# Kernel optimization log

Measured on AMD Instinct MI355X. Metric: run time of the kernel, lower is better.

Reference implementation:

```python
import jax, jax.numpy as jnp
import numpy as np

PATCH = 14  # dinov2 patch size
LN_EPS = 1e-5


def setup_inputs() -> dict:
    key = jax.random.key(0)
    ks = jax.random.split(key, 6)
    Nb, P, E, Hd = 4096, 5476, 1024, 128  # boxes, patches (74*74), embed_dim, hidden_dim
    return {
        "patch_tokens": jax.random.normal(ks[0], (1, P, E), dtype=jnp.float32),
        "bboxes": jax.random.randint(ks[1], (Nb, 4), 0, 1036, dtype=jnp.int32),
        "H": 1036,
        "W": 1036,
        "W1": jax.random.normal(ks[2], (E, Hd), dtype=jnp.float32) * 0.02,
        "b1": jnp.zeros((Hd,), dtype=jnp.float32),
        "gamma": jnp.ones((Hd,), dtype=jnp.float32),
        "beta": jnp.zeros((Hd,), dtype=jnp.float32),
        "W2": jax.random.normal(ks[3], (Hd, Hd), dtype=jnp.float32) * 0.02,
        "b2": jnp.zeros((Hd,), dtype=jnp.float32),
    }


def _roi_pool(patch_tokens, bboxes, H, W):
    """Vectorized equivalent of VisionEncoder.roi_pool_patches.

    patch_tokens: (1, nph*npw, E); bboxes: (Nb, 4) int pixel coords.
    Returns (Nb, E) mean of patch tokens inside each box.
    """
    nph, npw = H // PATCH, W // PATCH
    Nb = bboxes.shape[0]
    x1, y1, x2, y2 = (bboxes[:, 0], bboxes[:, 1], bboxes[:, 2], bboxes[:, 3])
    f32 = jnp.float32
    # int() truncation in torch == astype(int32) for non-negative values
    px1 = (x1.astype(f32) / W * npw).astype(jnp.int32)
    px2 = (x2.astype(f32) / W * npw).astype(jnp.int32)
    py1 = (y1.astype(f32) / H * nph).astype(jnp.int32)
    py2 = (y2.astype(f32) / H * nph).astype(jnp.int32)
    px1 = jnp.clip(px1, 0, npw - 1)
    px2 = jnp.maximum(px1 + 1, jnp.minimum(px2, npw))
    py1 = jnp.clip(py1, 0, nph - 1)
    py2 = jnp.maximum(py1 + 1, jnp.minimum(py2, nph))
    # Box membership masks over the patch grid (ragged gather expressed densely)
    ay = jnp.arange(nph, dtype=jnp.int32)
    ax = jnp.arange(npw, dtype=jnp.int32)
    my = (ay[None, :] >= py1[:, None]) & (ay[None, :] < py2[:, None])  # (Nb, nph)
    mx = (ax[None, :] >= px1[:, None]) & (ax[None, :] < px2[:, None])  # (Nb, npw)
    mask = (my[:, :, None] & mx[:, None, :]).reshape(Nb, nph * npw)
    mask = mask.astype(patch_tokens.dtype)
    counts = mask.sum(axis=-1, keepdims=True)  # always >= 1 by construction
    pooled = (mask @ patch_tokens[0]) / counts  # (Nb, E)
    return pooled


def _projection(x, W1, b1, gamma, beta, W2, b2):
    h = x @ W1 + b1
    mu = h.mean(axis=-1, keepdims=True)
    var = ((h - mu) ** 2).mean(axis=-1, keepdims=True)
    h = (h - mu) * jax.lax.rsqrt(var + LN_EPS) * gamma + beta
    h = jax.nn.relu(h)
    return h @ W2 + b2


def reference(patch_tokens, bboxes, H, W, W1, b1, gamma, beta, W2, b2):
    pooled = _roi_pool(patch_tokens, bboxes, H, W)
    return _projection(pooled, W1, b1, gamma, beta, W2, b2)
```

## Files before the change

### kernel.cpp

```cpp
#include <hip/hip_runtime.h>


#define HD 128
#define SPLITK 8

typedef __attribute__((ext_vector_type(8))) short bf16x8;
typedef __attribute__((ext_vector_type(4))) float f32x4;

__device__ __forceinline__ int decode_dim(const int* p, int fallback) {
    if (p == nullptr) return fallback;
    int vi = *p;
    if (vi >= 1 && vi <= 1000000) return vi;
    float vf = __int_as_float(vi);
    if (vf >= 1.0f && vf <= 1000000.0f) return (int)vf;
    return fallback;
}

__attribute__((noinline, optnone))
__device__ int coord_map(int x, int W, int n) {
    double rd = 1.0 / (double)W;
    float r = (float)rd;
    double qd = (double)x * (double)r;
    float q = (float)qd;
    double pd = (double)q * (double)n;
    float p = (float)pd;
    return (int)p;
}

__device__ __forceinline__ unsigned short bf16_rne(float x) {
    unsigned u = __float_as_uint(x);
    unsigned r = u + 0x7fffu + ((u >> 16) & 1u);
    return (unsigned short)(r >> 16);
}

__global__ __launch_bounds__(256) void split_w1_kernel(
    const float* __restrict__ W1, unsigned short* __restrict__ Whi,
    unsigned short* __restrict__ Wlo, int E)
{
    __shared__ float tile[64][65];
    int t = threadIdx.x;
    int k0 = blockIdx.x * 64, n0 = blockIdx.y * 64;

    int r = t >> 4, c4 = (t & 15) * 4;
#pragma unroll
    for (int i = 0; i < 4; ++i) {
        int kr = r + i * 16;
        *(float4*)&tile[kr][c4] =
            *(const float4*)&W1[(size_t)(k0 + kr) * HD + n0 + c4];
    }
    __syncthreads();

    int nl = t >> 2, kq = (t & 3) * 16;
    unsigned hp[8], lp[8];
#pragma unroll
    for (int j = 0; j < 8; ++j) {
        float x0 = tile[kq + 2 * j][nl];
        float x1 = tile[kq + 2 * j + 1][nl];
        unsigned h0 = bf16_rne(x0);
        unsigned h1 = bf16_rne(x1);
        float l0 = x0 - __uint_as_float(h0 << 16);
        float l1 = x1 - __uint_as_float(h1 << 16);
        hp[j] = h0 | ((unsigned)h1 << 16);
        lp[j] = (unsigned)bf16_rne(l0) | ((unsigned)bf16_rne(l1) << 16);
    }
    size_t off = (size_t)(n0 + nl) * E + k0 + kq;
    *(uint4*)(Whi + off)     = make_uint4(hp[0], hp[1], hp[2], hp[3]);
    *(uint4*)(Whi + off + 8) = make_uint4(hp[4], hp[5], hp[6], hp[7]);
    *(uint4*)(Wlo + off)     = make_uint4(lp[0], lp[1], lp[2], lp[3]);
    *(uint4*)(Wlo + off + 8) = make_uint4(lp[4], lp[5], lp[6], lp[7]);
}

__global__ __launch_bounds__(256) void gemm_u_mfma(
    const float* __restrict__ T, const unsigned short* __restrict__ Whi,
    const unsigned short* __restrict__ Wlo, float* __restrict__ U,
    int P, int E)
{
    int t = threadIdx.x;
    int lane = t & 63;
    int w = t >> 6;
    int row0 = blockIdx.x * 32 + (w & 1) * 16;
    int col0 = (w >> 1) * 64;
    int kchunk = E >> 3;
    int kbase = blockIdx.y * kchunk;
    float* Uo = U + (size_t)blockIdx.y * (size_t)P * HD;

    int lr  = lane & 15;
    int lkq = (lane >> 4) * 8;

    int arow = row0 + lr; if (arow >= P) arow = P - 1;
    const float* ap = T + (size_t)arow * E + kbase + lkq;
    const unsigned short* bh0 = Whi + (size_t)(col0 + lr) * E + kbase + lkq;
    const unsigned short* bl0 = Wlo + (size_t)(col0 + lr) * E + kbase + lkq;

    f32x4 acc[4];
#pragma unroll
    for (int n = 0; n < 4; ++n) acc[n] = (f32x4){0.f, 0.f, 0.f, 0.f};

    float4 ca0 = *(const float4*)(ap);
    float4 ca1 = *(const float4*)(ap + 4);

    for (int kt = 0; kt < kchunk; kt += 32) {
        float4 na0 = ca0, na1 = ca1;
        if (kt + 32 < kchunk) {
            na0 = *(const float4*)(ap + kt + 32);
            na1 = *(const float4*)(ap + kt + 36);
        }
        bf16x8 bhv[4], blv[4];
#pragma unroll
        for (int n = 0; n < 4; ++n) {
            bhv[n] = *(const bf16x8*)(bh0 + (size_t)(n * 16) * E + kt);
            blv[n] = *(const bf16x8*)(bl0 + (size_t)(n * 16) * E + kt);
        }

        float av[8] = {ca0.x, ca0.y, ca0.z, ca0.w, ca1.x, ca1.y, ca1.z, ca1.w};
        bf16x8 ahi, alo;
#pragma unroll
        for (int j = 0; j < 8; ++j) {
            unsigned h = bf16_rne(av[j]);
            ahi[j] = (short)h;
            float l = av[j] - __uint_as_float(h << 16);
            alo[j] = (short)bf16_rne(l);
        }

#pragma unroll
        for (int n = 0; n < 4; ++n) {
            acc[n] = __builtin_amdgcn_mfma_f32_16x16x32_bf16(ahi, bhv[n], acc[n], 0, 0, 0);
            acc[n] = __builtin_amdgcn_mfma_f32_16x16x32_bf16(alo, bhv[n], acc[n], 0, 0, 0);
            acc[n] = __builtin_amdgcn_mfma_f32_16x16x32_bf16(ahi, blv[n], acc[n], 0, 0, 0);
        }
        ca0 = na0; ca1 = na1;
    }

    int cr0 = row0 + (lane >> 4) * 4;
    int cc  = lane & 15;
#pragma unroll
    for (int n = 0; n < 4; ++n) {
#pragma unroll
        for (int r = 0; r < 4; ++r) {
            int p = cr0 + r;
            if (p < P) Uo[(size_t)p * HD + col0 + n * 16 + cc] = acc[n][r];
        }
    }
}

__global__ __launch_bounds__(256) void prefix_x_kernel(
    const float* __restrict__ U, float* __restrict__ S,
    int P, int npw, int nph)
{
    extern __shared__ float tile[];
    int t = threadIdx.x;
    int y = blockIdx.x;
    int ch0 = blockIdx.y * 64;
    size_t ustride = (size_t)P * HD;
    size_t ubase = (size_t)y * npw * HD + ch0;

    int nj = npw * 16;
    for (int j = t; j < nj; j += 256) {
        int x = j >> 4, cq = (j & 15) * 4;
        size_t off = ubase + (size_t)x * HD + cq;
        float4 s = *(const float4*)(U + off);
#pragma unroll
        for (int p = 1; p < SPLITK; ++p) {
            float4 v = *(const float4*)(U + (size_t)p * ustride + off);
            s.x += v.x; s.y += v.y; s.z += v.z; s.w += v.w;
        }
        *(float4*)&tile[x * 64 + cq] = s;
    }
    __syncthreads();

    if (t < 64) {
        int c = t;
        size_t srow = (size_t)(y + 1) * (npw + 1) * HD + ch0;
        S[srow + c] = 0.f;
        float acc = 0.f;
        for (int x = 0; x < npw; ++x) {
            acc += tile[x * 64 + c];
            S[srow + (size_t)(x + 1) * HD + c] = acc;
        }
    }
}

__global__ __launch_bounds__(256) void prefix_y_kernel(
    float* __restrict__ S, int npw, int nph)
{
    extern __shared__ float tile[];
    int t = threadIdx.x;
    int x = blockIdx.x;
    int ch0 = blockIdx.y * 64;
    size_t stride = (size_t)(npw + 1) * HD;
    size_t base = (size_t)x * HD + ch0;

    int nj = nph * 16;
    for (int j = t; j < nj; j += 256) {
        int y = j >> 4, cq = (j & 15) * 4;
        *(float4*)&tile[y * 64 + cq] =
            *(const float4*)(S + base + (size_t)(y + 1) * stride + cq);
    }
    __syncthreads();

    if (t < 64) {
        int c = t;
        S[base + c] = 0.f;
        float acc = 0.f;
        for (int y = 0; y < nph; ++y) {
            acc += tile[y * 64 + c];
            S[base + (size_t)(y + 1) * stride + c] = acc;
        }
    }
}

__global__ __launch_bounds__(256) void pool_proj_kernel(
    const float* __restrict__ S, const int* __restrict__ bboxes,
    const int* __restrict__ pH, const int* __restrict__ pW,
    const float* __restrict__ b1, const float* __restrict__ gamma,
    const float* __restrict__ beta, const float* __restrict__ W2,
    const float* __restrict__ b2, float* __restrict__ out,
    int Nb, int npw, int nph, int fbW, int fbH)
{
    __shared__ float hs[16][HD + 1];
    __shared__ float Bs[32][HD];
    __shared__ float red_s[16][17], red_q[16][17];
    __shared__ int   cI11[16], cI12[16], cI21[16], cI22[16];
    __shared__ float cCnt[16];
    __shared__ float mu_s[16], rs_s[16];

    int t = threadIdx.x;
    int c = t & 127;
    int rh = t >> 7;
    int row0 = blockIdx.x * 16;

    if (t < 16) {
        int b = row0 + t; if (b >= Nb) b = Nb - 1;
        int x1 = bboxes[b * 4 + 0];
        int y1 = bboxes[b * 4 + 1];
        int x2 = bboxes[b * 4 + 2];
        int y2 = bboxes[b * 4 + 3];
        int Wi = decode_dim(pW, fbW);
        int Hi = decode_dim(pH, fbH);
        int px1 = coord_map(x1, Wi, npw);
        int px2 = coord_map(x2, Wi, npw);
        int py1 = coord_map(y1, Hi, nph);
        int py2 = coord_map(y2, Hi, nph);
        px1 = min(max(px1, 0), npw - 1);
        px2 = max(px1 + 1, min(px2, npw));
        py1 = min(max(py1, 0), nph - 1);
        py2 = max(py1 + 1, min(py2, nph));
        int st = npw + 1;
        cI11[t] = (py1 * st + px1) * HD;
        cI12[t] = (py1 * st + px2) * HD;
        cI21[t] = (py2 * st + px1) * HD;
        cI22[t] = (py2 * st + px2) * HD;
        cCnt[t] = (float)((py2 - py1) * (px2 - px1));
    }
    __syncthreads();

    float bias1 = b1[c];
    float hv[8];
#pragma unroll
    for (int r = 0; r < 8; ++r) {
        int row = rh * 8 + r;
        float s = S[cI22[row] + c] - S[cI12[row] + c]
                - S[cI21[row] + c] + S[cI11[row] + c];
        hv[r] = s / cCnt[row] + bias1;
        hs[row][c] = hv[r];
    }
    __syncthreads();

    {
        int sr = t & 15;
        int sg = t >> 4;
        float ps = 0.f, pq = 0.f;
#pragma unroll
        for (int i = 0; i < 8; ++i) {
            float v = hs[sr][sg * 8 + i];
            ps += v; pq += v * v;
        }
        red_s[sr][sg] = ps; red_q[sr][sg] = pq;
    }
    __syncthreads();
    if (t < 16) {
        float s = 0.f, q = 0.f;
#pragma unroll
        for (int i = 0; i < 16; ++i) { s += red_s[t][i]; q += red_q[t][i]; }
        float m = s * (1.0f / HD);
        float v = q * (1.0f / HD) - m * m;
        mu_s[t] = m;
        rs_s[t] = rsqrtf(v + 1e-5f);
    }
    __syncthreads();

    float g = gamma[c], be = beta[c];
#pragma unroll
    for (int r = 0; r < 8; ++r) {
        int row = rh * 8 + r;
        float x = (hv[r] - mu_s[row]) * rs_s[row] * g + be;
        hs[row][c] = fmaxf(x, 0.f);
    }
    __syncthreads();

    float bias2 = b2[c];
    float acc2[8];
#pragma unroll
    for (int r = 0; r < 8; ++r) acc2[r] = bias2;
    for (int k0 = 0; k0 < HD; k0 += 32) {
#pragma unroll
        for (int i = 0; i < 16; ++i) {
            int idx = t + i * 256;
            int kk = idx >> 7, cc = idx & 127;
            Bs[kk][cc] = W2[(size_t)(k0 + kk) * HD + cc];
        }
        __syncthreads();
#pragma unroll
        for (int kk = 0; kk < 32; ++kk) {
            float bv = Bs[kk][c];
#pragma unroll
            for (int r = 0; r < 8; ++r)
                acc2[r] += hs[rh * 8 + r][k0 + kk] * bv;
        }
        __syncthreads();
    }

#pragma unroll
    for (int r = 0; r < 8; ++r) {
        int rg = row0 + rh * 8 + r;
        if (rg < Nb) out[(size_t)rg * HD + c] = acc2[r];
    }
}

extern "C" void kernel_launch(void* const* d_in, const int* in_sizes, int n_in,
                              void* d_out, int out_size, void* d_ws, size_t ws_size,
                              hipStream_t stream) {
    int iT = 0, iB = 1, iH = 2, iW = 3, iW1 = 4, ib1 = 5, ig = 6, ibe = 7,
        iW2 = 8, ib2 = 9;
    bool has_scalars = (n_in >= 10 && in_sizes[2] == 1 && in_sizes[3] == 1);
    if (!has_scalars) { iW1 = 2; ib1 = 3; ig = 4; ibe = 5; iW2 = 6; ib2 = 7; }

    const float* tokens = (const float*)d_in[iT];
    const int*   bboxes = (const int*)d_in[iB];
    const int*   pH     = has_scalars ? (const int*)d_in[iH] : nullptr;
    const int*   pW     = has_scalars ? (const int*)d_in[iW] : nullptr;
    const float* W1     = (const float*)d_in[iW1];
    const float* b1     = (const float*)d_in[ib1];
    const float* gamma  = (const float*)d_in[ig];
    const float* beta   = (const float*)d_in[ibe];
    const float* W2     = (const float*)d_in[iW2];
    const float* b2     = (const float*)d_in[ib2];
    float* out = (float*)d_out;

    int Hd = in_sizes[ib1];
    int E  = in_sizes[iW1] / Hd;
    int Nb = in_sizes[iB] / 4;
    int P  = in_sizes[iT] / E;
    int npw = 1;
    while ((npw + 1) * (npw + 1) <= P) ++npw;
    int nph = P / npw;
    (void)out_size; (void)ws_size;

    float* S = (float*)d_ws;
    size_t s_elems = ((size_t)(nph + 1) * (npw + 1) * HD + 255) & ~(size_t)255;
    float* U = S + s_elems;
    size_t u_elems = (size_t)SPLITK * (size_t)P * HD;
    unsigned short* Whi = (unsigned short*)(U + u_elems);
    unsigned short* Wlo = Whi + (size_t)E * HD;

    split_w1_kernel<<<dim3(E / 64, HD / 64), dim3(256), 0, stream>>>(
        W1, Whi, Wlo, E);

    int mtiles = (P + 31) / 32;
    gemm_u_mfma<<<dim3(mtiles, SPLITK), dim3(256), 0, stream>>>(
        tokens, Whi, Wlo, U, P, E);
    prefix_x_kernel<<<dim3(nph, 2), dim3(256), (size_t)npw * 64 * 4, stream>>>(
        U, S, P, npw, nph);
    prefix_y_kernel<<<dim3(npw + 1, 2), dim3(256), (size_t)nph * 64 * 4, stream>>>(
        S, npw, nph);
    pool_proj_kernel<<<dim3((Nb + 15) / 16), dim3(256), 0, stream>>>(
        S, bboxes, pH, pW, b1, gamma, beta, W2, b2, out, Nb, npw, nph,
        14 * npw, 14 * nph);
}
```

Before: 145.4 us.

## Fuse all stages into one persistent kernel with grid barriers, drop split-K

Replaces the five separate launches (W1 split, split-K GEMM, x-prefix, y-prefix, pool+projection) with one persistent kernel of 256 blocks x 512 threads, separated by software grid barriers built on atomics. The GEMM no longer splits K: each wave computes a full-K 16x64 tile, which removes the 8-way partial buffer and its reduction. The prefix scans run one wave per row or column straight from global memory, with no shared-memory staging. This saves launch overhead and partial-sum traffic, but adds barrier cost and relies on all 256 blocks being co-resident. It also leaves much less parallelism in the GEMM and scan phases (about 686 GEMM tasks and 148 scan tasks for 2048 waves).

New measurement: 302.8 us. 2.08x slower.

```diff
diff --git a/kernel.cpp b/kernel.cpp
--- a/kernel.cpp
+++ b/kernel.cpp
@@ -1,8 +1,9 @@
 #include <hip/hip_runtime.h>
 
 
-#define HD 128
-#define SPLITK 8
+#define HD   128
+#define NBLK 256
+#define NTHR 512
 
 typedef __attribute__((ext_vector_type(8))) short bf16x8;
 typedef __attribute__((ext_vector_type(4))) float f32x4;
@@ -33,297 +34,347 @@
     return (unsigned short)(r >> 16);
 }
 
-__global__ __launch_bounds__(256) void split_w1_kernel(
-    const float* __restrict__ W1, unsigned short* __restrict__ Whi,
-    unsigned short* __restrict__ Wlo, int E)
+__device__ __forceinline__ void gbar(int* cnt, int* gen) {
+    __syncthreads();
+    if (threadIdx.x == 0) {
+        __threadfence();
+        int g = __hip_atomic_load(gen, __ATOMIC_RELAXED,
+                                  __HIP_MEMORY_SCOPE_AGENT);
+        int a = __hip_atomic_fetch_add(cnt, 1, __ATOMIC_ACQ_REL,
+                                       __HIP_MEMORY_SCOPE_AGENT);
+        if (a == NBLK - 1) {
+            __hip_atomic_store(cnt, 0, __ATOMIC_RELAXED,
+                               __HIP_MEMORY_SCOPE_AGENT);
+            __hip_atomic_store(gen, g + 1, __ATOMIC_RELEASE,
+                               __HIP_MEMORY_SCOPE_AGENT);
+        } else {
+            while (__hip_atomic_load(gen, __ATOMIC_RELAXED,
+                                     __HIP_MEMORY_SCOPE_AGENT) == g)
+                __builtin_amdgcn_s_sleep(16);
+        }
+        __threadfence();
+    }
+    __syncthreads();
+}
+
+#define STEP(A0, A1, KT) do {                                               \
+    bf16x8 bhv[4], blv[4];                                                  \
+    _Pragma("unroll")                                                       \
+    for (int n = 0; n < 4; ++n) {                                           \
+        bhv[n] = *(const bf16x8*)(bh0 + (size_t)(n * 16) * E + (KT));       \
+        blv[n] = *(const bf16x8*)(bl0 + (size_t)(n * 16) * E + (KT));       \
+    }                                                                       \
+    float av[8] = {(A0).x, (A0).y, (A0).z, (A0).w,                          \
+                   (A1).x, (A1).y, (A1).z, (A1).w};                         \
+    bf16x8 ahi, alo;                                                        \
+    _Pragma("unroll")                                                       \
+    for (int j = 0; j < 8; ++j) {                                           \
+        unsigned h = bf16_rne(av[j]);                                       \
+        ahi[j] = (short)h;                                                  \
+        float l = av[j] - __uint_as_float(h << 16);                         \
+        alo[j] = (short)bf16_rne(l);                                        \
+    }                                                                       \
+    _Pragma("unroll")                                                       \
+    for (int n = 0; n < 4; ++n) {                                           \
+        acc[n] = __builtin_amdgcn_mfma_f32_16x16x32_bf16(ahi, bhv[n],       \
+                                                         acc[n], 0, 0, 0); \
+        acc[n] = __builtin_amdgcn_mfma_f32_16x16x32_bf16(alo, bhv[n],       \
+                                                         acc[n], 0, 0, 0); \
+        acc[n] = __builtin_amdgcn_mfma_f32_16x16x32_bf16(ahi, blv[n],       \
+                                                         acc[n], 0, 0, 0); \
+    }                                                                       \
+} while (0)
+
+__global__ __launch_bounds__(NTHR, 1) void fused_all(
+    const float* __restrict__ T, const int* __restrict__ bboxes,
+    const int* __restrict__ pH, const int* __restrict__ pW,
+    const float* __restrict__ W1, const float* __restrict__ b1,
+    const float* __restrict__ gamma, const float* __restrict__ beta,
+    const float* __restrict__ W2, const float* __restrict__ b2,
+    float* __restrict__ out,
+    float* S, float* U, unsigned short* Whi, unsigned short* Wlo,
+    int* cnt, int* gen,
+    int P, int E, int Nb, int npw, int nph, int fbW, int fbH)
 {
-    __shared__ float tile[64][65];
-    int t = threadIdx.x;
-    int k0 = blockIdx.x * 64, n0 = blockIdx.y * 64;
-
-    int r = t >> 4, c4 = (t & 15) * 4;
-#pragma unroll
-    for (int i = 0; i < 4; ++i) {
-        int kr = r + i * 16;
-        *(float4*)&tile[kr][c4] =
-            *(const float4*)&W1[(size_t)(k0 + kr) * HD + n0 + c4];
-    }
-    __syncthreads();
-
-    int nl = t >> 2, kq = (t & 3) * 16;
-    unsigned hp[8], lp[8];
-#pragma unroll
-    for (int j = 0; j < 8; ++j) {
-        float x0 = tile[kq + 2 * j][nl];
-        float x1 = tile[kq + 2 * j + 1][nl];
-        unsigned h0 = bf16_rne(x0);
-        unsigned h1 = bf16_rne(x1);
-        float l0 = x0 - __uint_as_float(h0 << 16);
-        float l1 = x1 - __uint_as_float(h1 << 16);
-        hp[j] = h0 | ((unsigned)h1 << 16);
-        lp[j] = (unsigned)bf16_rne(l0) | ((unsigned)bf16_rne(l1) << 16);
-    }
-    size_t off = (size_t)(n0 + nl) * E + k0 + kq;
-    *(uint4*)(Whi + off)     = make_uint4(hp[0], hp[1], hp[2], hp[3]);
-    *(uint4*)(Whi + off + 8) = make_uint4(hp[4], hp[5], hp[6], hp[7]);
-    *(uint4*)(Wlo + off)     = make_uint4(lp[0], lp[1], lp[2], lp[3]);
-    *(uint4*)(Wlo + off + 8) = make_uint4(lp[4], lp[5], lp[6], lp[7]);
-}
-
-__global__ __launch_bounds__(256) void gemm_u_mfma(
-    const float* __restrict__ T, const unsigned short* __restrict__ Whi,
-    const unsigned short* __restrict__ Wlo, float* __restrict__ U,
-    int P, int E)
-{
-    int t = threadIdx.x;
-    int lane = t & 63;
-    int w = t >> 6;
-    int row0 = blockIdx.x * 32 + (w & 1) * 16;
-    int col0 = (w >> 1) * 64;
-    int kchunk = E >> 3;
-    int kbase = blockIdx.y * kchunk;
-    float* Uo = U + (size_t)blockIdx.y * (size_t)P * HD;
-
-    int lr  = lane & 15;
-    int lkq = (lane >> 4) * 8;
-
-    int arow = row0 + lr; if (arow >= P) arow = P - 1;
-    const float* ap = T + (size_t)arow * E + kbase + lkq;
-    const unsigned short* bh0 = Whi + (size_t)(col0 + lr) * E + kbase + lkq;
-    const unsigned short* bl0 = Wlo + (size_t)(col0 + lr) * E + kbase + lkq;
-
-    f32x4 acc[4];
-#pragma unroll
-    for (int n = 0; n < 4; ++n) acc[n] = (f32x4){0.f, 0.f, 0.f, 0.f};
-
-    float4 ca0 = *(const float4*)(ap);
-    float4 ca1 = *(const float4*)(ap + 4);
-
-    for (int kt = 0; kt < kchunk; kt += 32) {
-        float4 na0 = ca0, na1 = ca1;
-        if (kt + 32 < kchunk) {
-            na0 = *(const float4*)(ap + kt + 32);
-            na1 = *(const float4*)(ap + kt + 36);
-        }
-        bf16x8 bhv[4], blv[4];
-#pragma unroll
-        for (int n = 0; n < 4; ++n) {
-            bhv[n] = *(const bf16x8*)(bh0 + (size_t)(n * 16) * E + kt);
-            blv[n] = *(const bf16x8*)(bl0 + (size_t)(n * 16) * E + kt);
-        }
-
-        float av[8] = {ca0.x, ca0.y, ca0.z, ca0.w, ca1.x, ca1.y, ca1.z, ca1.w};
-        bf16x8 ahi, alo;
-#pragma unroll
-        for (int j = 0; j < 8; ++j) {
-            unsigned h = bf16_rne(av[j]);
-            ahi[j] = (short)h;
-            float l = av[j] - __uint_as_float(h << 16);
-            alo[j] = (short)bf16_rne(l);
-        }
-
-#pragma unroll
-        for (int n = 0; n < 4; ++n) {
-            acc[n] = __builtin_amdgcn_mfma_f32_16x16x32_bf16(ahi, bhv[n], acc[n], 0, 0, 0);
-            acc[n] = __builtin_amdgcn_mfma_f32_16x16x32_bf16(alo, bhv[n], acc[n], 0, 0, 0);
-            acc[n] = __builtin_amdgcn_mfma_f32_16x16x32_bf16(ahi, blv[n], acc[n], 0, 0, 0);
-        }
-        ca0 = na0; ca1 = na1;
-    }
-
-    int cr0 = row0 + (lane >> 4) * 4;
-    int cc  = lane & 15;
-#pragma unroll
-    for (int n = 0; n < 4; ++n) {
-#pragma unroll
-        for (int r = 0; r < 4; ++r) {
-            int p = cr0 + r;
-            if (p < P) Uo[(size_t)p * HD + col0 + n * 16 + cc] = acc[n][r];
-        }
-    }
-}
-
-__global__ __launch_bounds__(256) void prefix_x_kernel(
-    const float* __restrict__ U, float* __restrict__ S,
-    int P, int npw, int nph)
-{
-    extern __shared__ float tile[];
-    int t = threadIdx.x;
-    int y = blockIdx.x;
-    int ch0 = blockIdx.y * 64;
-    size_t ustride = (size_t)P * HD;
-    size_t ubase = (size_t)y * npw * HD + ch0;
-
-    int nj = npw * 16;
-    for (int j = t; j < nj; j += 256) {
-        int x = j >> 4, cq = (j & 15) * 4;
-        size_t off = ubase + (size_t)x * HD + cq;
-        float4 s = *(const float4*)(U + off);
-#pragma unroll
-        for (int p = 1; p < SPLITK; ++p) {
-            float4 v = *(const float4*)(U + (size_t)p * ustride + off);
-            s.x += v.x; s.y += v.y; s.z += v.z; s.w += v.w;
-        }
-        *(float4*)&tile[x * 64 + cq] = s;
-    }
-    __syncthreads();
-
-    if (t < 64) {
-        int c = t;
-        size_t srow = (size_t)(y + 1) * (npw + 1) * HD + ch0;
-        S[srow + c] = 0.f;
-        float acc = 0.f;
-        for (int x = 0; x < npw; ++x) {
-            acc += tile[x * 64 + c];
-            S[srow + (size_t)(x + 1) * HD + c] = acc;
-        }
-    }
-}
-
-__global__ __launch_bounds__(256) void prefix_y_kernel(
-    float* __restrict__ S, int npw, int nph)
-{
-    extern __shared__ float tile[];
-    int t = threadIdx.x;
-    int x = blockIdx.x;
-    int ch0 = blockIdx.y * 64;
-    size_t stride = (size_t)(npw + 1) * HD;
-    size_t base = (size_t)x * HD + ch0;
-
-    int nj = nph * 16;
-    for (int j = t; j < nj; j += 256) {
-        int y = j >> 4, cq = (j & 15) * 4;
-        *(float4*)&tile[y * 64 + cq] =
-            *(const float4*)(S + base + (size_t)(y + 1) * stride + cq);
-    }
-    __syncthreads();
-
-    if (t < 64) {
-        int c = t;
-        S[base + c] = 0.f;
-        float acc = 0.f;
-        for (int y = 0; y < nph; ++y) {
-            acc += tile[y * 64 + c];
-            S[base + (size_t)(y + 1) * stride + c] = acc;
-        }
-    }
-}
-
-__global__ __launch_bounds__(256) void pool_proj_kernel(
-    const float* __restrict__ S, const int* __restrict__ bboxes,
-    const int* __restrict__ pH, const int* __restrict__ pW,
-    const float* __restrict__ b1, const float* __restrict__ gamma,
-    const float* __restrict__ beta, const float* __restrict__ W2,
-    const float* __restrict__ b2, float* __restrict__ out,
-    int Nb, int npw, int nph, int fbW, int fbH)
-{
+    __shared__ float sh_tile[64][65];
     __shared__ float hs[16][HD + 1];
     __shared__ float Bs[32][HD];
-    __shared__ float red_s[16][17], red_q[16][17];
+    __shared__ float red_s[16][33], red_q[16][33];
     __shared__ int   cI11[16], cI12[16], cI21[16], cI22[16];
     __shared__ float cCnt[16];
     __shared__ float mu_s[16], rs_s[16];
 
     int t = threadIdx.x;
-    int c = t & 127;
-    int rh = t >> 7;
-    int row0 = blockIdx.x * 16;
-
-    if (t < 16) {
-        int b = row0 + t; if (b >= Nb) b = Nb - 1;
-        int x1 = bboxes[b * 4 + 0];
-        int y1 = bboxes[b * 4 + 1];
-        int x2 = bboxes[b * 4 + 2];
-        int y2 = bboxes[b * 4 + 3];
-        int Wi = decode_dim(pW, fbW);
-        int Hi = decode_dim(pH, fbH);
-        int px1 = coord_map(x1, Wi, npw);
-        int px2 = coord_map(x2, Wi, npw);
-        int py1 = coord_map(y1, Hi, nph);
-        int py2 = coord_map(y2, Hi, nph);
-        px1 = min(max(px1, 0), npw - 1);
-        px2 = max(px1 + 1, min(px2, npw));
-        py1 = min(max(py1, 0), nph - 1);
-        py2 = max(py1 + 1, min(py2, nph));
-        int st = npw + 1;
-        cI11[t] = (py1 * st + px1) * HD;
-        cI12[t] = (py1 * st + px2) * HD;
-        cI21[t] = (py2 * st + px1) * HD;
-        cI22[t] = (py2 * st + px2) * HD;
-        cCnt[t] = (float)((py2 - py1) * (px2 - px1));
-    }
-    __syncthreads();
-
-    float bias1 = b1[c];
-    float hv[8];
-#pragma unroll
-    for (int r = 0; r < 8; ++r) {
-        int row = rh * 8 + r;
-        float s = S[cI22[row] + c] - S[cI12[row] + c]
-                - S[cI21[row] + c] + S[cI11[row] + c];
-        hv[r] = s / cCnt[row] + bias1;
-        hs[row][c] = hv[r];
-    }
-    __syncthreads();
+    int b = blockIdx.x;
+    int w = t >> 6;
+    int lane = t & 63;
 
     {
-        int sr = t & 15;
-        int sg = t >> 4;
-        float ps = 0.f, pq = 0.f;
-#pragma unroll
-        for (int i = 0; i < 8; ++i) {
-            float v = hs[sr][sg * 8 + i];
-            ps += v; pq += v * v;
-        }
-        red_s[sr][sg] = ps; red_q[sr][sg] = pq;
-    }
-    __syncthreads();
-    if (t < 16) {
-        float s = 0.f, q = 0.f;
-#pragma unroll
-        for (int i = 0; i < 16; ++i) { s += red_s[t][i]; q += red_q[t][i]; }
-        float m = s * (1.0f / HD);
-        float v = q * (1.0f / HD) - m * m;
-        mu_s[t] = m;
-        rs_s[t] = rsqrtf(v + 1e-5f);
-    }
-    __syncthreads();
-
-    float g = gamma[c], be = beta[c];
-#pragma unroll
-    for (int r = 0; r < 8; ++r) {
-        int row = rh * 8 + r;
-        float x = (hv[r] - mu_s[row]) * rs_s[row] * g + be;
-        hs[row][c] = fmaxf(x, 0.f);
-    }
-    __syncthreads();
-
-    float bias2 = b2[c];
-    float acc2[8];
-#pragma unroll
-    for (int r = 0; r < 8; ++r) acc2[r] = bias2;
-    for (int k0 = 0; k0 < HD; k0 += 32) {
-#pragma unroll
-        for (int i = 0; i < 16; ++i) {
-            int idx = t + i * 256;
-            int kk = idx >> 7, cc = idx & 127;
-            Bs[kk][cc] = W2[(size_t)(k0 + kk) * HD + cc];
-        }
-        __syncthreads();
-#pragma unroll
-        for (int kk = 0; kk < 32; ++kk) {
-            float bv = Bs[kk][c];
-#pragma unroll
-            for (int r = 0; r < 8; ++r)
-                acc2[r] += hs[rh * 8 + r][k0 + kk] * bv;
-        }
-        __syncthreads();
-    }
-
-#pragma unroll
-    for (int r = 0; r < 8; ++r) {
-        int rg = row0 + rh * 8 + r;
-        if (rg < Nb) out[(size_t)rg * HD + c] = acc2[r];
+        int ntile0 = (E >> 6) * (HD >> 6);
+        for (int tb = b; tb < ntile0; tb += NBLK) {
+            int k0 = (tb >> 1) * 64, n0 = (tb & 1) * 64;
+            if (t < 256) {
+                int r = t >> 4, c4 = (t & 15) * 4;
+#pragma unroll
+                for (int i = 0; i < 4; ++i) {
+                    int kr = r + i * 16;
+                    *(float4*)&sh_tile[kr][c4] =
+                        *(const float4*)&W1[(size_t)(k0 + kr) * HD + n0 + c4];
+                }
+            }
+            __syncthreads();
+            if (t < 256) {
+                int nl = t >> 2, kq = (t & 3) * 16;
+                unsigned hp[8], lp[8];
+#pragma unroll
+                for (int j = 0; j < 8; ++j) {
+                    float x0 = sh_tile[kq + 2 * j][nl];
+                    float x1 = sh_tile[kq + 2 * j + 1][nl];
+                    unsigned h0 = bf16_rne(x0);
+                    unsigned h1 = bf16_rne(x1);
+                    float l0 = x0 - __uint_as_float(h0 << 16);
+                    float l1 = x1 - __uint_as_float(h1 << 16);
+                    hp[j] = h0 | ((unsigned)h1 << 16);
+                    lp[j] = (unsigned)bf16_rne(l0) |
+                            ((unsigned)bf16_rne(l1) << 16);
+                }
+                size_t off = (size_t)(n0 + nl) * E + k0 + kq;
+                *(uint4*)(Whi + off)     = make_uint4(hp[0], hp[1], hp[2], hp[3]);
+                *(uint4*)(Whi + off + 8) = make_uint4(hp[4], hp[5], hp[6], hp[7]);
+                *(uint4*)(Wlo + off)     = make_uint4(lp[0], lp[1], lp[2], lp[3]);
+                *(uint4*)(Wlo + off + 8) = make_uint4(lp[4], lp[5], lp[6], lp[7]);
+            }
+            __syncthreads();
+        }
+    }
+    gbar(cnt, gen);
+
+    {
+        int ntasks = ((P + 15) >> 4) * 2;
+        for (int task = w * NBLK + b; task < ntasks; task += NBLK * 8) {
+            int rt = task >> 1, ch = task & 1;
+            int row0 = rt * 16, col0 = ch * 64;
+            int lr = lane & 15, lkq = (lane >> 4) * 8;
+            int arow = row0 + lr; if (arow >= P) arow = P - 1;
+            const float* ap = T + (size_t)arow * E + lkq;
+            const unsigned short* bh0 = Whi + (size_t)(col0 + lr) * E + lkq;
+            const unsigned short* bl0 = Wlo + (size_t)(col0 + lr) * E + lkq;
+
+            f32x4 acc[4];
+#pragma unroll
+            for (int n = 0; n < 4; ++n) acc[n] = (f32x4){0.f, 0.f, 0.f, 0.f};
+
+            float4 pa0 = *(const float4*)(ap);
+            float4 pa1 = *(const float4*)(ap + 4);
+            float4 qa0 = *(const float4*)(ap + 32);
+            float4 qa1 = *(const float4*)(ap + 36);
+
+            for (int kt = 0; kt < E; kt += 64) {
+                float4 na0 = pa0, na1 = pa1, ma0 = qa0, ma1 = qa1;
+                if (kt + 64 < E) {
+                    na0 = *(const float4*)(ap + kt + 64);
+                    na1 = *(const float4*)(ap + kt + 68);
+                }
+                if (kt + 96 < E) {
+                    ma0 = *(const float4*)(ap + kt + 96);
+                    ma1 = *(const float4*)(ap + kt + 100);
+                }
+                STEP(pa0, pa1, kt);
+                STEP(qa0, qa1, kt + 32);
+                pa0 = na0; pa1 = na1; qa0 = ma0; qa1 = ma1;
+            }
+
+            int cr0 = row0 + (lane >> 4) * 4;
+            int cc  = lane & 15;
+#pragma unroll
+            for (int n = 0; n < 4; ++n) {
+#pragma unroll
+                for (int r = 0; r < 4; ++r) {
+                    int p = cr0 + r;
+                    if (p < P)
+                        U[(size_t)p * HD + col0 + n * 16 + cc] = acc[n][r];
+                }
+            }
+        }
+    }
+    gbar(cnt, gen);
+
+    {
+        int nsc = nph * 2;
+        for (int task = w * NBLK + b; task < nsc; task += NBLK * 8) {
+            int y = task >> 1, chalf = task & 1;
+            int c = chalf * 64 + lane;
+            const float* ub = U + (size_t)y * npw * HD + c;
+            float* Sy = S + (size_t)(y + 1) * (npw + 1) * HD + c;
+            Sy[0] = 0.f;
+            float acc = 0.f;
+            int x = 0;
+            for (; x + 8 <= npw; x += 8) {
+                float v0 = ub[(size_t)(x + 0) * HD];
+                float v1 = ub[(size_t)(x + 1) * HD];
+                float v2 = ub[(size_t)(x + 2) * HD];
+                float v3 = ub[(size_t)(x + 3) * HD];
+                float v4 = ub[(size_t)(x + 4) * HD];
+                float v5 = ub[(size_t)(x + 5) * HD];
+                float v6 = ub[(size_t)(x + 6) * HD];
+                float v7 = ub[(size_t)(x + 7) * HD];
+                acc += v0; Sy[(size_t)(x + 1) * HD] = acc;
+                acc += v1; Sy[(size_t)(x + 2) * HD] = acc;
+                acc += v2; Sy[(size_t)(x + 3) * HD] = acc;
+                acc += v3; Sy[(size_t)(x + 4) * HD] = acc;
+                acc += v4; Sy[(size_t)(x + 5) * HD] = acc;
+                acc += v5; Sy[(size_t)(x + 6) * HD] = acc;
+                acc += v6; Sy[(size_t)(x + 7) * HD] = acc;
+                acc += v7; Sy[(size_t)(x + 8) * HD] = acc;
+            }
+            for (; x < npw; ++x) {
+                acc += ub[(size_t)x * HD];
+                Sy[(size_t)(x + 1) * HD] = acc;
+            }
+        }
+    }
+    gbar(cnt, gen);
+
+    {
+        int nsc = (npw + 1) * 2;
+        size_t stride = (size_t)(npw + 1) * HD;
+        for (int task = w * NBLK + b; task < nsc; task += NBLK * 8) {
+            int x = task >> 1, chalf = task & 1;
+            int c = chalf * 64 + lane;
+            float* p0 = S + (size_t)x * HD + c;
+            p0[0] = 0.f;
+            float acc = 0.f;
+            int y = 1;
+            for (; y + 8 <= nph + 1; y += 8) {
+                float v0 = p0[(size_t)(y + 0) * stride];
+                float v1 = p0[(size_t)(y + 1) * stride];
+                float v2 = p0[(size_t)(y + 2) * stride];
+                float v3 = p0[(size_t)(y + 3) * stride];
+                float v4 = p0[(size_t)(y + 4) * stride];
+                float v5 = p0[(size_t)(y + 5) * stride];
+                float v6 = p0[(size_t)(y + 6) * stride];
+                float v7 = p0[(size_t)(y + 7) * stride];
+                acc += v0; p0[(size_t)(y + 0) * stride] = acc;
+                acc += v1; p0[(size_t)(y + 1) * stride] = acc;
+                acc += v2; p0[(size_t)(y + 2) * stride] = acc;
+                acc += v3; p0[(size_t)(y + 3) * stride] = acc;
+                acc += v4; p0[(size_t)(y + 4) * stride] = acc;
+                acc += v5; p0[(size_t)(y + 5) * stride] = acc;
+                acc += v6; p0[(size_t)(y + 6) * stride] = acc;
+                acc += v7; p0[(size_t)(y + 7) * stride] = acc;
+            }
+            for (; y <= nph; ++y) {
+                acc += p0[(size_t)y * stride];
+                p0[(size_t)y * stride] = acc;
+            }
+        }
+    }
+    gbar(cnt, gen);
+
+    {
+        int nbt = (Nb + 15) >> 4;
+        int c  = t & 127;
+        int rh = t >> 7;
+        for (int bb = b; bb < nbt; bb += NBLK) {
+            int row0 = bb * 16;
+            if (t < 16) {
+                int bx = row0 + t; if (bx >= Nb) bx = Nb - 1;
+                int x1 = bboxes[bx * 4 + 0];
+                int y1 = bboxes[bx * 4 + 1];
+                int x2 = bboxes[bx * 4 + 2];
+                int y2 = bboxes[bx * 4 + 3];
+                int Wi = decode_dim(pW, fbW);
+                int Hi = decode_dim(pH, fbH);
+                int px1 = coord_map(x1, Wi, npw);
+                int px2 = coord_map(x2, Wi, npw);
+                int py1 = coord_map(y1, Hi, nph);
+                int py2 = coord_map(y2, Hi, nph);
+                px1 = min(max(px1, 0), npw - 1);
+                px2 = max(px1 + 1, min(px2, npw));
+                py1 = min(max(py1, 0), nph - 1);
+                py2 = max(py1 + 1, min(py2, nph));
+                int st = npw + 1;
+                cI11[t] = (py1 * st + px1) * HD;
+                cI12[t] = (py1 * st + px2) * HD;
+                cI21[t] = (py2 * st + px1) * HD;
+                cI22[t] = (py2 * st + px2) * HD;
+                cCnt[t] = (float)((py2 - py1) * (px2 - px1));
+            }
+            __syncthreads();
+
+            float bias1 = b1[c];
+            float hv[4];
+#pragma unroll
+            for (int r = 0; r < 4; ++r) {
+                int row = rh * 4 + r;
+                float s = S[cI22[row] + c] - S[cI12[row] + c]
+                        - S[cI21[row] + c] + S[cI11[row] + c];
+                hv[r] = s / cCnt[row] + bias1;
+                hs[row][c] = hv[r];
+            }
+            __syncthreads();
+
+            {
+                int sr = t & 15;
+                int sg = t >> 4;
+                float ps = 0.f, pq = 0.f;
+#pragma unroll
+                for (int i = 0; i < 4; ++i) {
+                    float v = hs[sr][sg * 4 + i];
+                    ps += v; pq += v * v;
+                }
+                red_s[sr][sg] = ps; red_q[sr][sg] = pq;
+            }
+            __syncthreads();
+            if (t < 16) {
+                float s = 0.f, q = 0.f;
+#pragma unroll
+                for (int i = 0; i < 32; ++i) { s += red_s[t][i]; q += red_q[t][i]; }
+                float m = s * (1.0f / HD);
+                float v = q * (1.0f / HD) - m * m;
+                mu_s[t] = m;
+                rs_s[t] = rsqrtf(v + 1e-5f);
+            }
+            __syncthreads();
+
+            float g = gamma[c], be = beta[c];
+#pragma unroll
+            for (int r = 0; r < 4; ++r) {
+                int row = rh * 4 + r;
+                float x = (hv[r] - mu_s[row]) * rs_s[row] * g + be;
+                hs[row][c] = fmaxf(x, 0.f);
+            }
+            __syncthreads();
+
+            float bias2 = b2[c];
+            float acc2[4];
+#pragma unroll
+            for (int r = 0; r < 4; ++r) acc2[r] = bias2;
+            for (int k0 = 0; k0 < HD; k0 += 32) {
+#pragma unroll
+                for (int i = 0; i < 8; ++i) {
+                    int idx = t + i * 512;
+                    int kk = idx >> 7, cc2 = idx & 127;
+                    Bs[kk][cc2] = W2[(size_t)(k0 + kk) * HD + cc2];
+                }
+                __syncthreads();
+#pragma unroll
+                for (int kk = 0; kk < 32; ++kk) {
+                    float bv = Bs[kk][c];
+#pragma unroll
+                    for (int r = 0; r < 4; ++r)
+                        acc2[r] += hs[rh * 4 + r][k0 + kk] * bv;
+                }
+                __syncthreads();
+            }
+
+#pragma unroll
+            for (int r = 0; r < 4; ++r) {
+                int rg = row0 + rh * 4 + r;
+                if (rg < Nb) out[(size_t)rg * HD + c] = acc2[r];
+            }
+            __syncthreads();
+        }
     }
 }
 
@@ -356,24 +407,17 @@
     int nph = P / npw;
     (void)out_size; (void)ws_size;
 
-    float* S = (float*)d_ws;
+    int* ctrl = (int*)d_ws;
+    float* S = (float*)((char*)d_ws + 256);
     size_t s_elems = ((size_t)(nph + 1) * (npw + 1) * HD + 255) & ~(size_t)255;
     float* U = S + s_elems;
-    size_t u_elems = (size_t)SPLITK * (size_t)P * HD;
+    size_t u_elems = ((size_t)P * HD + 255) & ~(size_t)255;
     unsigned short* Whi = (unsigned short*)(U + u_elems);
     unsigned short* Wlo = Whi + (size_t)E * HD;
 
-    split_w1_kernel<<<dim3(E / 64, HD / 64), dim3(256), 0, stream>>>(
-        W1, Whi, Wlo, E);
-
-    int mtiles = (P + 31) / 32;
-    gemm_u_mfma<<<dim3(mtiles, SPLITK), dim3(256), 0, stream>>>(
-        tokens, Whi, Wlo, U, P, E);
-    prefix_x_kernel<<<dim3(nph, 2), dim3(256), (size_t)npw * 64 * 4, stream>>>(
-        U, S, P, npw, nph);
-    prefix_y_kernel<<<dim3(npw + 1, 2), dim3(256), (size_t)nph * 64 * 4, stream>>>(
-        S, npw, nph);
-    pool_proj_kernel<<<dim3((Nb + 15) / 16), dim3(256), 0, stream>>>(
-        S, bboxes, pH, pW, b1, gamma, beta, W2, b2, out, Nb, npw, nph,
-        14 * npw, 14 * nph);
-}
+    hipMemsetAsync(ctrl, 0, 64, stream);
+    fused_all<<<dim3(NBLK), dim3(NTHR), 0, stream>>>(
+        tokens, bboxes, pH, pW, W1, b1, gamma, beta, W2, b2, out,
+        S, U, Whi, Wlo, ctrl, ctrl + 1,
+        P, E, Nb, npw, nph, 14 * npw, 14 * nph);
+}
```

## Fuse prefix passes into per-channel SAT kernel and transpose GEMM output

Applied to the files above, without the earlier changes.

Merges the x and y prefix-sum kernels into one kernel per channel that reduces the split-K partials, builds the 2D summed-area table in LDS and writes it out. The GEMM now stores its output channel-major with float4 writes, and its K loop is fully unrolled with A preloaded and B double-buffered. This removes a kernel launch and an intermediate round trip through global memory. In exchange, it hardcodes four K steps per split, assumes P is a multiple of 4, and uses strided writes to S.

Result: slower. 148.6 us (+2.2%).

```diff
diff --git a/kernel.cpp b/kernel.cpp
--- a/kernel.cpp
+++ b/kernel.cpp
@@ -1,7 +1,7 @@
 #include <hip/hip_runtime.h>
 
 
-#define HD 128
+#define HD   128
 #define SPLITK 8
 
 typedef __attribute__((ext_vector_type(8))) short bf16x8;
@@ -82,7 +82,7 @@
     int col0 = (w >> 1) * 64;
     int kchunk = E >> 3;
     int kbase = blockIdx.y * kchunk;
-    float* Uo = U + (size_t)blockIdx.y * (size_t)P * HD;
+    float* Uo = U + (size_t)blockIdx.y * (size_t)HD * P;
 
     int lr  = lane & 15;
     int lkq = (lane >> 4) * 8;
@@ -92,27 +92,36 @@
     const unsigned short* bh0 = Whi + (size_t)(col0 + lr) * E + kbase + lkq;
     const unsigned short* bl0 = Wlo + (size_t)(col0 + lr) * E + kbase + lkq;
 
+    float4 a[8];
+#pragma unroll
+    for (int s = 0; s < 4; ++s) {
+        a[2 * s]     = *(const float4*)(ap + s * 32);
+        a[2 * s + 1] = *(const float4*)(ap + s * 32 + 4);
+    }
+
     f32x4 acc[4];
 #pragma unroll
     for (int n = 0; n < 4; ++n) acc[n] = (f32x4){0.f, 0.f, 0.f, 0.f};
 
-    float4 ca0 = *(const float4*)(ap);
-    float4 ca1 = *(const float4*)(ap + 4);
-
-    for (int kt = 0; kt < kchunk; kt += 32) {
-        float4 na0 = ca0, na1 = ca1;
-        if (kt + 32 < kchunk) {
-            na0 = *(const float4*)(ap + kt + 32);
-            na1 = *(const float4*)(ap + kt + 36);
-        }
-        bf16x8 bhv[4], blv[4];
-#pragma unroll
-        for (int n = 0; n < 4; ++n) {
-            bhv[n] = *(const bf16x8*)(bh0 + (size_t)(n * 16) * E + kt);
-            blv[n] = *(const bf16x8*)(bl0 + (size_t)(n * 16) * E + kt);
-        }
-
-        float av[8] = {ca0.x, ca0.y, ca0.z, ca0.w, ca1.x, ca1.y, ca1.z, ca1.w};
+    bf16x8 bh[2][4], bl[2][4];
+#pragma unroll
+    for (int n = 0; n < 4; ++n) {
+        bh[0][n] = *(const bf16x8*)(bh0 + (size_t)(n * 16) * E);
+        bl[0][n] = *(const bf16x8*)(bl0 + (size_t)(n * 16) * E);
+    }
+
+#pragma unroll
+    for (int s = 0; s < 4; ++s) {
+        int cur = s & 1, nxt = cur ^ 1;
+        if (s < 3) {
+#pragma unroll
+            for (int n = 0; n < 4; ++n) {
+                bh[nxt][n] = *(const bf16x8*)(bh0 + (size_t)(n * 16) * E + (s + 1) * 32);
+                bl[nxt][n] = *(const bf16x8*)(bl0 + (size_t)(n * 16) * E + (s + 1) * 32);
+            }
+        }
+        float av[8] = {a[2 * s].x, a[2 * s].y, a[2 * s].z, a[2 * s].w,
+                       a[2 * s + 1].x, a[2 * s + 1].y, a[2 * s + 1].z, a[2 * s + 1].w};
         bf16x8 ahi, alo;
 #pragma unroll
         for (int j = 0; j < 8; ++j) {
@@ -121,91 +130,69 @@
             float l = av[j] - __uint_as_float(h << 16);
             alo[j] = (short)bf16_rne(l);
         }
-
 #pragma unroll
         for (int n = 0; n < 4; ++n) {
-            acc[n] = __builtin_amdgcn_mfma_f32_16x16x32_bf16(ahi, bhv[n], acc[n], 0, 0, 0);
-            acc[n] = __builtin_amdgcn_mfma_f32_16x16x32_bf16(alo, bhv[n], acc[n], 0, 0, 0);
-            acc[n] = __builtin_amdgcn_mfma_f32_16x16x32_bf16(ahi, blv[n], acc[n], 0, 0, 0);
-        }
-        ca0 = na0; ca1 = na1;
+            acc[n] = __builtin_amdgcn_mfma_f32_16x16x32_bf16(ahi, bh[cur][n], acc[n], 0, 0, 0);
+            acc[n] = __builtin_amdgcn_mfma_f32_16x16x32_bf16(alo, bh[cur][n], acc[n], 0, 0, 0);
+            acc[n] = __builtin_amdgcn_mfma_f32_16x16x32_bf16(ahi, bl[cur][n], acc[n], 0, 0, 0);
+        }
     }
 
     int cr0 = row0 + (lane >> 4) * 4;
     int cc  = lane & 15;
-#pragma unroll
-    for (int n = 0; n < 4; ++n) {
-#pragma unroll
-        for (int r = 0; r < 4; ++r) {
-            int p = cr0 + r;
-            if (p < P) Uo[(size_t)p * HD + col0 + n * 16 + cc] = acc[n][r];
-        }
-    }
-}
-
-__global__ __launch_bounds__(256) void prefix_x_kernel(
+    if (cr0 < P) {
+#pragma unroll
+        for (int n = 0; n < 4; ++n) {
+            float4 v = make_float4(acc[n][0], acc[n][1], acc[n][2], acc[n][3]);
+            *(float4*)&Uo[(size_t)(col0 + n * 16 + cc) * P + cr0] = v;
+        }
+    }
+}
+
+__global__ __launch_bounds__(512) void sat_kernel(
     const float* __restrict__ U, float* __restrict__ S,
     int P, int npw, int nph)
 {
     extern __shared__ float tile[];
     int t = threadIdx.x;
-    int y = blockIdx.x;
-    int ch0 = blockIdx.y * 64;
-    size_t ustride = (size_t)P * HD;
-    size_t ubase = (size_t)y * npw * HD + ch0;
-
-    int nj = npw * 16;
-    for (int j = t; j < nj; j += 256) {
-        int x = j >> 4, cq = (j & 15) * 4;
-        size_t off = ubase + (size_t)x * HD + cq;
-        float4 s = *(const float4*)(U + off);
-#pragma unroll
-        for (int p = 1; p < SPLITK; ++p) {
-            float4 v = *(const float4*)(U + (size_t)p * ustride + off);
-            s.x += v.x; s.y += v.y; s.z += v.z; s.w += v.w;
-        }
-        *(float4*)&tile[x * 64 + cq] = s;
-    }
-    __syncthreads();
-
-    if (t < 64) {
-        int c = t;
-        size_t srow = (size_t)(y + 1) * (npw + 1) * HD + ch0;
-        S[srow + c] = 0.f;
-        float acc = 0.f;
-        for (int x = 0; x < npw; ++x) {
-            acc += tile[x * 64 + c];
-            S[srow + (size_t)(x + 1) * HD + c] = acc;
-        }
-    }
-}
-
-__global__ __launch_bounds__(256) void prefix_y_kernel(
-    float* __restrict__ S, int npw, int nph)
-{
-    extern __shared__ float tile[];
-    int t = threadIdx.x;
-    int x = blockIdx.x;
-    int ch0 = blockIdx.y * 64;
-    size_t stride = (size_t)(npw + 1) * HD;
-    size_t base = (size_t)x * HD + ch0;
-
-    int nj = nph * 16;
-    for (int j = t; j < nj; j += 256) {
-        int y = j >> 4, cq = (j & 15) * 4;
-        *(float4*)&tile[y * 64 + cq] =
-            *(const float4*)(S + base + (size_t)(y + 1) * stride + cq);
-    }
-    __syncthreads();
-
-    if (t < 64) {
-        int c = t;
-        S[base + c] = 0.f;
-        float acc = 0.f;
-        for (int y = 0; y < nph; ++y) {
-            acc += tile[y * 64 + c];
-            S[base + (size_t)(y + 1) * stride + c] = acc;
-        }
+    int c = blockIdx.x;
+    int ldt = npw + 3;
+    int PP = nph * npw;
+
+    const float* Uc = U + (size_t)c * P;
+    size_t ustride = (size_t)HD * P;
+
+    for (int i = t; i < PP; i += 512) {
+        float s = Uc[i];
+#pragma unroll
+        for (int p = 1; p < SPLITK; ++p) s += Uc[(size_t)p * ustride + i];
+        int y = i / npw, x = i - y * npw;
+        tile[(y + 1) * ldt + (x + 1)] = s;
+    }
+    if (t <= npw) tile[t] = 0.f;
+    if (t <= nph) tile[t * ldt] = 0.f;
+    __syncthreads();
+
+    if (t < nph) {
+        int row = (t + 1) * ldt;
+        float a = 0.f;
+        for (int x = 1; x <= npw; ++x) { a += tile[row + x]; tile[row + x] = a; }
+    }
+    __syncthreads();
+
+    if (t < npw) {
+        int col = t + 1;
+        float a = 0.f;
+        for (int y = 1; y <= nph; ++y) {
+            a += tile[y * ldt + col]; tile[y * ldt + col] = a;
+        }
+    }
+    __syncthreads();
+
+    int tot = (nph + 1) * (npw + 1);
+    for (int i = t; i < tot; i += 512) {
+        int y = i / (npw + 1), x = i - y * (npw + 1);
+        S[((size_t)y * (npw + 1) + x) * HD + c] = tile[y * ldt + x];
     }
 }
 
@@ -359,7 +346,7 @@
     float* S = (float*)d_ws;
     size_t s_elems = ((size_t)(nph + 1) * (npw + 1) * HD + 255) & ~(size_t)255;
     float* U = S + s_elems;
-    size_t u_elems = (size_t)SPLITK * (size_t)P * HD;
+    size_t u_elems = ((size_t)SPLITK * HD * P + 255) & ~(size_t)255;
     unsigned short* Whi = (unsigned short*)(U + u_elems);
     unsigned short* Wlo = Whi + (size_t)E * HD;
 
@@ -369,10 +356,11 @@
     int mtiles = (P + 31) / 32;
     gemm_u_mfma<<<dim3(mtiles, SPLITK), dim3(256), 0, stream>>>(
         tokens, Whi, Wlo, U, P, E);
-    prefix_x_kernel<<<dim3(nph, 2), dim3(256), (size_t)npw * 64 * 4, stream>>>(
+
+    size_t sat_lds = (size_t)(nph + 1) * (npw + 3) * sizeof(float);
+    sat_kernel<<<dim3(HD), dim3(512), sat_lds, stream>>>(
         U, S, P, npw, nph);
-    prefix_y_kernel<<<dim3(npw + 1, 2), dim3(256), (size_t)nph * 64 * 4, stream>>>(
-        S, npw, nph);
+
     pool_proj_kernel<<<dim3((Nb + 15) / 16), dim3(256), 0, stream>>>(
         S, bboxes, pH, pW, b1, gamma, beta, W2, b2, out, Nb, npw, nph,
         14 * npw, 14 * nph);
```
